# Kernel tuning notes

Hardware: AMD Instinct MI355X
Metric: run time of the kernel (lower is better)

## Reference

```python
import jax, jax.numpy as jnp
import numpy as np

N_NODES = 50000
N_EDGES = 800000


def _sage_conv(h, ei, W_l, W_r, b_l):
    """PyG SAGEConv: lin_l(mean_{j->i} h_j) + lin_r(h_i). lin_l has bias, lin_r does not."""
    src, dst = ei[0], ei[1]
    # mean-aggregate raw features first (linear commutes with mean) to avoid [E, out] intermediates
    msum = jax.ops.segment_sum(h[src], dst, num_segments=N_NODES)          # [N, d]
    cnt = jax.ops.segment_sum(jnp.ones((ei.shape[1], 1), h.dtype), dst,
                              num_segments=N_NODES)                         # [N, 1]
    mean = msum / jnp.maximum(cnt, 1.0)
    return mean @ W_l + b_l + h @ W_r


def setup_inputs() -> dict:
    key = jax.random.key(0)
    ks = jax.random.split(key, 8)
    d_in, d_hid, d_out = 64, 64, 32
    return {
        "x": jax.random.normal(ks[0], (N_NODES, d_in), dtype=jnp.float32),
        "ei0": jax.random.randint(ks[1], (2, N_EDGES), 0, N_NODES, dtype=jnp.int32),
        "ei1": jax.random.randint(ks[2], (2, N_EDGES), 0, N_NODES, dtype=jnp.int32),
        "Wl": jax.random.normal(ks[3], (2, 2, d_in, d_hid), dtype=jnp.float32) * 0.05,
        "Wr": jax.random.normal(ks[4], (2, 2, d_in, d_hid), dtype=jnp.float32) * 0.05,
        "bl": jax.random.normal(ks[5], (2, 2, d_hid), dtype=jnp.float32) * 0.05,
        "lin_W": jax.random.normal(ks[6], (d_hid, d_out), dtype=jnp.float32) * 0.05,
        "lin_b": jax.random.normal(ks[7], (d_out,), dtype=jnp.float32) * 0.05,
    }


def reference(x, ei0, ei1, Wl, Wr, bl, lin_W, lin_b):
    edge_indices = (ei0, ei1)  # one edge_index per relation
    h = x
    for l in range(2):  # layers (structurally fixed)
        out = None
        for r, ei in enumerate(edge_indices):  # HeteroConv aggr='sum' over relations
            y = _sage_conv(h, ei, Wl[l, r], Wr[l, r], bl[l, r])
            out = y if out is None else out + y
        h = jax.nn.relu(out)
    return h @ lin_W + lin_b
```

## Files before the change

### kernel.cpp

```cpp
#include <hip/hip_runtime.h>

#define NN 50000
#define CAP 32
#define OVF_CAP 4096
#define SHARD_W 64
#define NSH 782
#define NPB 512

__device__ __forceinline__ unsigned short f2bf(float f) {
    unsigned u = __float_as_uint(f);
    u += 0x7fffu + ((u >> 16) & 1u);
    return (unsigned short)(u >> 16);
}
__device__ __forceinline__ float bf2f(unsigned short u) {
    return __uint_as_float(((unsigned)u) << 16);
}

__global__ __launch_bounds__(256) void init_fuse(
    const float* __restrict__ in, unsigned short* __restrict__ out, int n4,
    int* __restrict__ zbuf, int nint)
{
    int stride = gridDim.x * blockDim.x;
    int id0 = blockIdx.x * blockDim.x + threadIdx.x;
    for (int i = id0; i < n4; i += stride) {
        float4 v = ((const float4*)in)[i];
        ushort4 o;
        o.x = f2bf(v.x); o.y = f2bf(v.y); o.z = f2bf(v.z); o.w = f2bf(v.w);
        ((ushort4*)out)[i] = o;
    }
    for (int i = id0; i < nint; i += stride) zbuf[i] = 0;
}


__global__ __launch_bounds__(256) void shard_hist(
    const int* __restrict__ ei0, int E0,
    const int* __restrict__ ei1, int E1,
    unsigned short* __restrict__ hist16)
{
    __shared__ unsigned lh[NSH];
    int local = blockIdx.x; int rel = 0;
    if (local >= NPB) { local -= NPB; rel = 1; }
    int pb = (local & 7) * (NPB / 8) + (local >> 3);
    const int* ei = rel ? ei1 : ei0;
    int E         = rel ? E1  : E0;
    int ce = (E + NPB - 1) / NPB;
    int lo = pb * ce, hi = min(lo + ce, E);

    for (int i = threadIdx.x; i < NSH; i += 256) lh[i] = 0;
    __syncthreads();
    for (int t = lo + threadIdx.x; t < hi; t += 256)
        atomicAdd(&lh[ei[E + t] >> 6], 1u);
    __syncthreads();
    for (int i = threadIdx.x; i < NSH; i += 256)
        hist16[((size_t)rel * NSH + i) * NPB + pb] = (unsigned short)lh[i];
}

__global__ __launch_bounds__(256) void total_pass(
    const unsigned short* __restrict__ hist16, int* __restrict__ tot)
{
    int gw = (blockIdx.x * 256 + threadIdx.x) >> 6;
    int lane = threadIdx.x & 63;
    if (gw >= 2 * NSH) return;
    uint4 v = ((const uint4*)(hist16 + (size_t)gw * NPB))[lane];
    unsigned s = (v.x & 0xffffu) + (v.x >> 16) + (v.y & 0xffffu) + (v.y >> 16)
               + (v.z & 0xffffu) + (v.z >> 16) + (v.w & 0xffffu) + (v.w >> 16);
    for (int off = 32; off; off >>= 1) s += __shfl_down(s, off);
    if (lane == 0) tot[gw] = (int)s;
}

__global__ __launch_bounds__(256) void scan_pass(
    const int* __restrict__ tot, int* __restrict__ sbase)
{
    __shared__ int ps[256];
    int t = threadIdx.x;
    int v[7];
    int s = 0;
    #pragma unroll
    for (int j = 0; j < 7; j++) {
        int i = t * 7 + j;
        v[j] = (i < 2 * NSH) ? tot[i] : 0;
        s += v[j];
    }
    ps[t] = s;
    __syncthreads();
    for (int off = 1; off < 256; off <<= 1) {
        int add = (t >= off) ? ps[t - off] : 0;
        __syncthreads();
        ps[t] += add;
        __syncthreads();
    }
    int run = (t == 0) ? 0 : ps[t - 1];
    #pragma unroll
    for (int j = 0; j < 7; j++) {
        int i = t * 7 + j;
        if (i < 2 * NSH) sbase[i] = run;
        run += v[j];
    }
    if (t == 255) sbase[2 * NSH] = run;
}

__global__ __launch_bounds__(256) void blockbase_pass(
    const unsigned short* __restrict__ hist16, const int* __restrict__ sbase,
    unsigned* __restrict__ pbase)
{
    int gw = (blockIdx.x * 256 + threadIdx.x) >> 6;
    int lane = threadIdx.x & 63;
    if (gw >= 2 * NSH) return;
    uint4 v = ((const uint4*)(hist16 + (size_t)gw * NPB))[lane];
    unsigned c[8] = {v.x & 0xffffu, v.x >> 16, v.y & 0xffffu, v.y >> 16,
                     v.z & 0xffffu, v.z >> 16, v.w & 0xffffu, v.w >> 16};
    unsigned lsum = 0;
    #pragma unroll
    for (int j = 0; j < 8; j++) lsum += c[j];
    unsigned incl = lsum;
    for (int off = 1; off < 64; off <<= 1) {
        unsigned n = __shfl_up(incl, off);
        if (lane >= off) incl += n;
    }
    unsigned run = (unsigned)sbase[gw] + incl - lsum;
    unsigned* prow = pbase + (size_t)gw * NPB + lane * 8;
    #pragma unroll
    for (int j = 0; j < 8; j++) { prow[j] = run; run += c[j]; }
}

__global__ __launch_bounds__(256) void partition_pass(
    const int* __restrict__ ei0, int E0,
    const int* __restrict__ ei1, int E1,
    const unsigned* __restrict__ pbase,
    unsigned* __restrict__ compact)
{
    __shared__ unsigned lbase[NSH];
    __shared__ unsigned lrank[NSH];
    int local = blockIdx.x; int rel = 0;
    if (local >= NPB) { local -= NPB; rel = 1; }
    int pb = (local & 7) * (NPB / 8) + (local >> 3);
    const int* ei = rel ? ei1 : ei0;
    int E         = rel ? E1  : E0;
    int ce = (E + NPB - 1) / NPB;
    int lo = pb * ce, hi = min(lo + ce, E);

    for (int i = threadIdx.x; i < NSH; i += 256) {
        lbase[i] = pbase[((size_t)rel * NSH + i) * NPB + pb];
        lrank[i] = 0;
    }
    __syncthreads();
    for (int t = lo + threadIdx.x; t < hi; t += 256) {
        int dst = ei[E + t];
        int src = ei[t];
        int s = dst >> 6;
        unsigned r = atomicAdd(&lrank[s], 1u);
        compact[lbase[s] + r] = ((unsigned)dst << 16) | (unsigned)src;
    }
}

__global__ __launch_bounds__(256) void bin_pass(
    const unsigned* __restrict__ compact, const int* __restrict__ sbase,
    unsigned short* __restrict__ bins, int* __restrict__ deg,
    int2* __restrict__ ovf, int* __restrict__ ovf_cnt)
{
    __shared__ unsigned lcnt[SHARD_W];
    int bid = blockIdx.x;
    int rel = bid / NSH;
    int s   = bid - rel * NSH;
    if (threadIdx.x < SHARD_W) lcnt[threadIdx.x] = 0;
    __syncthreads();
    int base = sbase[bid];
    int tot  = sbase[bid + 1] - base;
    int taskbase = rel * NN + s * SHARD_W;
    for (int j = threadIdx.x; j < tot; j += 256) {
        unsigned e = compact[base + j];
        int dst = (int)(e >> 16);
        int src = (int)(e & 0xffffu);
        int loc = dst & (SHARD_W - 1);
        unsigned r = atomicAdd(&lcnt[loc], 1u);
        int task = taskbase + loc;
        if (r < CAP) {
            bins[(size_t)task * CAP + r] = (unsigned short)src;
        } else {
            int o = atomicAdd(ovf_cnt, 1);
            if (o < OVF_CAP) ovf[o] = make_int2(task, src);
        }
    }
    __syncthreads();
    if (threadIdx.x < SHARD_W) {
        int node = s * SHARD_W + threadIdx.x;
        if (node < NN) deg[rel * NN + node] = (int)lcnt[threadIdx.x];
    }
}

__global__ __launch_bounds__(256) void aggregate(
    const unsigned short* __restrict__ bins, const int* __restrict__ deg,
    const unsigned short* __restrict__ hb, unsigned short* __restrict__ agg,
    const int2* __restrict__ ovf, const int* __restrict__ ovf_cnt)
{
    int lane = threadIdx.x & 63;
    int half = lane >> 5;
    int p = lane & 31;
    int wid = (blockIdx.x * blockDim.x + threadIdx.x) >> 6;
    int nwaves = (gridDim.x * blockDim.x) >> 6;
    const unsigned int* hb32 = (const unsigned int*)hb;
    unsigned int* agg32 = (unsigned int*)agg;

    for (int task = wid; task < 2 * NN; task += nwaves) {
        int d = deg[task];
        int m = min(d, CAP);
        int idx = 0;
        if (lane < m) idx = bins[(size_t)task * CAP + lane];
        float a00=0.f,a01=0.f, a10=0.f,a11=0.f, a20=0.f,a21=0.f, a30=0.f,a31=0.f;
        int F = m >> 1;
        int q = 0;
        for (; q + 4 <= F; q += 4) {
            int s0 = __shfl(idx, 2*(q+0) + half);
            int s1 = __shfl(idx, 2*(q+1) + half);
            int s2 = __shfl(idx, 2*(q+2) + half);
            int s3 = __shfl(idx, 2*(q+3) + half);
            unsigned u0 = hb32[(size_t)s0 * 32 + p];
            unsigned u1 = hb32[(size_t)s1 * 32 + p];
            unsigned u2 = hb32[(size_t)s2 * 32 + p];
            unsigned u3 = hb32[(size_t)s3 * 32 + p];
            a00 += __uint_as_float(u0 << 16); a01 += __uint_as_float(u0 & 0xffff0000u);
            a10 += __uint_as_float(u1 << 16); a11 += __uint_as_float(u1 & 0xffff0000u);
            a20 += __uint_as_float(u2 << 16); a21 += __uint_as_float(u2 & 0xffff0000u);
            a30 += __uint_as_float(u3 << 16); a31 += __uint_as_float(u3 & 0xffff0000u);
        }
        for (; q < F; ++q) {
            int s = __shfl(idx, 2*q + half);
            unsigned u = hb32[(size_t)s * 32 + p];
            a00 += __uint_as_float(u << 16); a01 += __uint_as_float(u & 0xffff0000u);
        }
        if (m & 1) {
            int s = __shfl(idx, m - 1);
            if (half == 0) {
                unsigned u = hb32[(size_t)s * 32 + p];
                a00 += __uint_as_float(u << 16); a01 += __uint_as_float(u & 0xffff0000u);
            }
        }
        if (d > CAP) {
            int cnt = min(*ovf_cnt, OVF_CAP);
            for (int e = 0; e < cnt; ++e) {
                int2 v = ovf[e];
                if (v.x == task && half == 0) {
                    unsigned u = hb32[(size_t)v.y * 32 + p];
                    a00 += __uint_as_float(u << 16); a01 += __uint_as_float(u & 0xffff0000u);
                }
            }
        }
        float s0 = (a00 + a10) + (a20 + a30);
        float s1 = (a01 + a11) + (a21 + a31);
        s0 += __shfl_xor(s0, 32);
        s1 += __shfl_xor(s1, 32);
        if (half == 0) {
            float inv = 1.0f / (float)max(d, 1);
            unsigned lo = (unsigned)f2bf(s0 * inv);
            unsigned hi = (unsigned)f2bf(s1 * inv);
            agg32[(size_t)task * 32 + p] = lo | (hi << 16);
        }
    }
}

#define RST 66
__global__ __launch_bounds__(256) void layer_gemm(
    const unsigned short* __restrict__ agg0, const unsigned short* __restrict__ agg1,
    const unsigned short* __restrict__ selfb,
    const float* __restrict__ Wl0, const float* __restrict__ Wl1,
    const float* __restrict__ Wr0, const float* __restrict__ Wr1,
    const float* __restrict__ b0, const float* __restrict__ b1,
    unsigned short* __restrict__ hb16)
{
    __shared__ float Wch[64 * 64];
    __shared__ float rowsT[64 * RST];
    __shared__ float bias[64];

    int tid = threadIdx.x;
    int base = blockIdx.x * 64;
    if (tid < 64) bias[tid] = b0[tid] + b1[tid];

    int j8 = (tid & 7) * 8;
    int n2 = (tid >> 3) * 2;

    float acc[2][8];
    #pragma unroll
    for (int i = 0; i < 2; i++)
        #pragma unroll
        for (int c = 0; c < 8; c++) acc[i][c] = 0.f;

    for (int chunk = 0; chunk < 3; chunk++) {
        const float* W = (chunk == 0) ? Wl0 : (chunk == 1) ? Wl1 : Wr0;
        const unsigned short* src = (chunk == 0) ? agg0 : (chunk == 1) ? agg1 : selfb;
        __syncthreads();
        #pragma unroll
        for (int r = 0; r < 4; r++) {
            int i = tid + 256 * r;
            float4 w = *(const float4*)&W[i * 4];
            if (chunk == 2) {
                float4 w2 = *(const float4*)&Wr1[i * 4];
                w.x += w2.x; w.y += w2.y; w.z += w2.z; w.w += w2.w;
            }
            *(float4*)&Wch[i * 4] = w;
        }
        #pragma unroll
        for (int r = 0; r < 4; r++) {
            int i = tid + 256 * r;
            int node = i >> 4;
            int k4 = (i & 15) * 4;
            int g = base + node;
            ushort4 u = make_ushort4(0, 0, 0, 0);
            if (g < NN) u = *(const ushort4*)&src[(size_t)g * 64 + k4];
            rowsT[(k4 + 0) * RST + node] = bf2f(u.x);
            rowsT[(k4 + 1) * RST + node] = bf2f(u.y);
            rowsT[(k4 + 2) * RST + node] = bf2f(u.z);
            rowsT[(k4 + 3) * RST + node] = bf2f(u.w);
        }
        __syncthreads();
        #pragma unroll 4
        for (int k = 0; k < 64; k++) {
            float4 wa = *(const float4*)&Wch[k * 64 + j8];
            float4 wb = *(const float4*)&Wch[k * 64 + j8 + 4];
            float2 rv = *(const float2*)&rowsT[k * RST + n2];
            float w[8] = {wa.x, wa.y, wa.z, wa.w, wb.x, wb.y, wb.z, wb.w};
            float rr[2] = {rv.x, rv.y};
            #pragma unroll
            for (int i = 0; i < 2; i++)
                #pragma unroll
                for (int c = 0; c < 8; c++)
                    acc[i][c] = fmaf(rr[i], w[c], acc[i][c]);
        }
    }

    #pragma unroll
    for (int i = 0; i < 2; i++) {
        int g = base + n2 + i;
        if (g < NN) {
            ushort4 p0, p1;
            p0.x = f2bf(fmaxf(acc[i][0] + bias[j8 + 0], 0.f));
            p0.y = f2bf(fmaxf(acc[i][1] + bias[j8 + 1], 0.f));
            p0.z = f2bf(fmaxf(acc[i][2] + bias[j8 + 2], 0.f));
            p0.w = f2bf(fmaxf(acc[i][3] + bias[j8 + 3], 0.f));
            p1.x = f2bf(fmaxf(acc[i][4] + bias[j8 + 4], 0.f));
            p1.y = f2bf(fmaxf(acc[i][5] + bias[j8 + 5], 0.f));
            p1.z = f2bf(fmaxf(acc[i][6] + bias[j8 + 6], 0.f));
            p1.w = f2bf(fmaxf(acc[i][7] + bias[j8 + 7], 0.f));
            *(ushort4*)&hb16[(size_t)g * 64 + j8]     = p0;
            *(ushort4*)&hb16[(size_t)g * 64 + j8 + 4] = p1;
        }
    }
}

__global__ __launch_bounds__(256) void layer_gemm_final(
    const unsigned short* __restrict__ agg0, const unsigned short* __restrict__ agg1,
    const unsigned short* __restrict__ selfb,
    const float* __restrict__ Wl0, const float* __restrict__ Wl1,
    const float* __restrict__ Wr0, const float* __restrict__ Wr1,
    const float* __restrict__ b0, const float* __restrict__ b1,
    const float* __restrict__ linW, const float* __restrict__ linb,
    float* __restrict__ out)
{
    __shared__ float Wch[64 * 64];
    __shared__ float rowsT[64 * RST];
    __shared__ float bias[64];

    int tid = threadIdx.x;
    int base = blockIdx.x * 64;
    if (tid < 64) bias[tid] = b0[tid] + b1[tid];

    int j8 = (tid & 7) * 8;
    int n2 = (tid >> 3) * 2;

    float acc[2][8];
    #pragma unroll
    for (int i = 0; i < 2; i++)
        #pragma unroll
        for (int c = 0; c < 8; c++) acc[i][c] = 0.f;

    for (int chunk = 0; chunk < 3; chunk++) {
        const float* W = (chunk == 0) ? Wl0 : (chunk == 1) ? Wl1 : Wr0;
        const unsigned short* src = (chunk == 0) ? agg0 : (chunk == 1) ? agg1 : selfb;
        __syncthreads();
        #pragma unroll
        for (int r = 0; r < 4; r++) {
            int i = tid + 256 * r;
            float4 w = *(const float4*)&W[i * 4];
            if (chunk == 2) {
                float4 w2 = *(const float4*)&Wr1[i * 4];
                w.x += w2.x; w.y += w2.y; w.z += w2.z; w.w += w2.w;
            }
            *(float4*)&Wch[i * 4] = w;
        }
        #pragma unroll
        for (int r = 0; r < 4; r++) {
            int i = tid + 256 * r;
            int node = i >> 4;
            int k4 = (i & 15) * 4;
            int g = base + node;
            ushort4 u = make_ushort4(0, 0, 0, 0);
            if (g < NN) u = *(const ushort4*)&src[(size_t)g * 64 + k4];
            rowsT[(k4 + 0) * RST + node] = bf2f(u.x);
            rowsT[(k4 + 1) * RST + node] = bf2f(u.y);
            rowsT[(k4 + 2) * RST + node] = bf2f(u.z);
            rowsT[(k4 + 3) * RST + node] = bf2f(u.w);
        }
        __syncthreads();
        #pragma unroll 4
        for (int k = 0; k < 64; k++) {
            float4 wa = *(const float4*)&Wch[k * 64 + j8];
            float4 wb = *(const float4*)&Wch[k * 64 + j8 + 4];
            float2 rv = *(const float2*)&rowsT[k * RST + n2];
            float w[8] = {wa.x, wa.y, wa.z, wa.w, wb.x, wb.y, wb.z, wb.w};
            float rr[2] = {rv.x, rv.y};
            #pragma unroll
            for (int i = 0; i < 2; i++)
                #pragma unroll
                for (int c = 0; c < 8; c++)
                    acc[i][c] = fmaf(rr[i], w[c], acc[i][c]);
        }
    }

    float o[2][8];
    #pragma unroll
    for (int i = 0; i < 2; i++)
        #pragma unroll
        for (int c = 0; c < 8; c++)
            o[i][c] = fmaxf(acc[i][c] + bias[j8 + c], 0.f);

    __syncthreads();

    #pragma unroll
    for (int r = 0; r < 2; r++) {
        int i = tid + 256 * r;
        *(float4*)&Wch[i * 4] = *(const float4*)&linW[i * 4];
    }
    if (tid < 32) bias[tid] = linb[tid];
    #pragma unroll
    for (int i = 0; i < 2; i++)
        #pragma unroll
        for (int c = 0; c < 8; c++)
            rowsT[(j8 + c) * RST + (n2 + i)] = o[i][c];
    __syncthreads();

    int j4 = (tid & 7) * 4;
    float acc2[2][4];
    #pragma unroll
    for (int i = 0; i < 2; i++)
        #pragma unroll
        for (int c = 0; c < 4; c++) acc2[i][c] = 0.f;
    #pragma unroll 4
    for (int k = 0; k < 64; k++) {
        float4 w = *(const float4*)&Wch[k * 32 + j4];
        float2 rv = *(const float2*)&rowsT[k * RST + n2];
        float wr[4] = {w.x, w.y, w.z, w.w};
        float rr[2] = {rv.x, rv.y};
        #pragma unroll
        for (int i = 0; i < 2; i++)
            #pragma unroll
            for (int c = 0; c < 4; c++)
                acc2[i][c] = fmaf(rr[i], wr[c], acc2[i][c]);
    }
    #pragma unroll
    for (int i = 0; i < 2; i++) {
        int g = base + n2 + i;
        if (g < NN) {
            float4 ov;
            ov.x = acc2[i][0] + bias[j4 + 0];
            ov.y = acc2[i][1] + bias[j4 + 1];
            ov.z = acc2[i][2] + bias[j4 + 2];
            ov.w = acc2[i][3] + bias[j4 + 3];
            *(float4*)&out[(size_t)g * 32 + j4] = ov;
        }
    }
}

extern "C" void kernel_launch(void* const* d_in, const int* in_sizes, int n_in,
                              void* d_out, int out_size, void* d_ws, size_t ws_size,
                              hipStream_t stream)
{
    const float* x    = (const float*)d_in[0];
    const int*   ei0  = (const int*)d_in[1];
    const int*   ei1  = (const int*)d_in[2];
    const float* Wl   = (const float*)d_in[3];
    const float* Wr   = (const float*)d_in[4];
    const float* bl   = (const float*)d_in[5];
    const float* linW = (const float*)d_in[6];
    const float* linb = (const float*)d_in[7];
    float* out = (float*)d_out;

    int E0 = in_sizes[1] / 2;
    int E1 = in_sizes[2] / 2;

    unsigned short* bins = (unsigned short*)d_ws;
    unsigned short* h1b  = bins + (size_t)2 * NN * CAP;
    unsigned short* aggb = h1b + (size_t)NN * 64;
    unsigned short* agg0 = aggb;
    unsigned short* agg1 = aggb + (size_t)NN * 64;
    unsigned short* xb   = aggb + (size_t)2 * NN * 64;
    int*  deg     = (int*)(xb + (size_t)NN * 64);
    int*  ovf_cnt = deg + 2 * NN;
    int2* ovf     = (int2*)(ovf_cnt + 8);

    unsigned*       compact = (unsigned*)h1b;
    unsigned short* hist16  = aggb;
    unsigned*       pbase   = (unsigned*)(aggb + (size_t)2 * NSH * NPB);
    int*            tot     = (int*)(aggb + (size_t)2 * NSH * NPB * 3);
    int*            sbase   = tot + 2 * NSH;

    dim3 blk(256);
    int ggrid = (NN + 63) / 64;
    int wave_grid = (2 * NSH * 64 + 255) / 256;

    init_fuse<<<1024, blk, 0, stream>>>(x, xb, NN * 16, ovf_cnt, 8);

    shard_hist<<<2 * NPB, blk, 0, stream>>>(ei0, E0, ei1, E1, hist16);
    total_pass<<<wave_grid, blk, 0, stream>>>(hist16, tot);
    scan_pass<<<1, blk, 0, stream>>>(tot, sbase);
    blockbase_pass<<<wave_grid, blk, 0, stream>>>(hist16, sbase, pbase);
    partition_pass<<<2 * NPB, blk, 0, stream>>>(ei0, E0, ei1, E1, pbase, compact);
    bin_pass<<<2 * NSH, blk, 0, stream>>>(compact, sbase, bins, deg, ovf, ovf_cnt);

    aggregate<<<4096, blk, 0, stream>>>(bins, deg, xb, aggb, ovf, ovf_cnt);
    layer_gemm<<<ggrid, blk, 0, stream>>>(agg0, agg1, xb,
        Wl + 0, Wl + 4096, Wr + 0, Wr + 4096, bl + 0, bl + 64, h1b);

    aggregate<<<4096, blk, 0, stream>>>(bins, deg, h1b, aggb, ovf, ovf_cnt);
    layer_gemm_final<<<ggrid, blk, 0, stream>>>(agg0, agg1, h1b,
        Wl + 8192, Wl + 12288, Wr + 8192, Wr + 12288, bl + 128, bl + 192,
        linW, linb, out);
}
```

Baseline: 245.8 us.

## Fuse binning preprocessing passes into one cooperative kernel with grid syncs

Merges the seven preprocessing kernels (bf16 conversion, histogram, totals, scan, block bases, partition, binning) into a single cooperative launch of 1024 blocks, with grid.sync() between phases. The aim is to remove the per-launch overhead and inter-kernel gaps of many small kernels. In exchange, each phase runs with a fixed grid (the bin phase loops over shards, total/blockbase use only part of the grid), the single-block scan leaves the rest of the grid idle at a barrier, and all 1024 blocks must be co-resident for the cooperative launch.

```diff
diff --git a/kernel.cpp b/kernel.cpp
--- a/kernel.cpp
+++ b/kernel.cpp
@@ -1,4 +1,7 @@
 #include <hip/hip_runtime.h>
+#include <hip/hip_cooperative_groups.h>
+
+namespace cg = cooperative_groups;
 
 #define NN 50000
 #define CAP 32
@@ -16,175 +19,173 @@
     return __uint_as_float(((unsigned)u) << 16);
 }
 
-__global__ __launch_bounds__(256) void init_fuse(
-    const float* __restrict__ in, unsigned short* __restrict__ out, int n4,
-    int* __restrict__ zbuf, int nint)
-{
-    int stride = gridDim.x * blockDim.x;
-    int id0 = blockIdx.x * blockDim.x + threadIdx.x;
-    for (int i = id0; i < n4; i += stride) {
-        float4 v = ((const float4*)in)[i];
-        ushort4 o;
-        o.x = f2bf(v.x); o.y = f2bf(v.y); o.z = f2bf(v.z); o.w = f2bf(v.w);
-        ((ushort4*)out)[i] = o;
-    }
-    for (int i = id0; i < nint; i += stride) zbuf[i] = 0;
-}
-
-
-__global__ __launch_bounds__(256) void shard_hist(
+__global__ __launch_bounds__(256) void binning_coop(
+    const float* __restrict__ x, unsigned short* __restrict__ xb,
     const int* __restrict__ ei0, int E0,
     const int* __restrict__ ei1, int E1,
-    unsigned short* __restrict__ hist16)
-{
-    __shared__ unsigned lh[NSH];
-    int local = blockIdx.x; int rel = 0;
-    if (local >= NPB) { local -= NPB; rel = 1; }
-    int pb = (local & 7) * (NPB / 8) + (local >> 3);
-    const int* ei = rel ? ei1 : ei0;
-    int E         = rel ? E1  : E0;
-    int ce = (E + NPB - 1) / NPB;
-    int lo = pb * ce, hi = min(lo + ce, E);
-
-    for (int i = threadIdx.x; i < NSH; i += 256) lh[i] = 0;
-    __syncthreads();
-    for (int t = lo + threadIdx.x; t < hi; t += 256)
-        atomicAdd(&lh[ei[E + t] >> 6], 1u);
-    __syncthreads();
-    for (int i = threadIdx.x; i < NSH; i += 256)
-        hist16[((size_t)rel * NSH + i) * NPB + pb] = (unsigned short)lh[i];
-}
-
-__global__ __launch_bounds__(256) void total_pass(
-    const unsigned short* __restrict__ hist16, int* __restrict__ tot)
-{
-    int gw = (blockIdx.x * 256 + threadIdx.x) >> 6;
-    int lane = threadIdx.x & 63;
-    if (gw >= 2 * NSH) return;
-    uint4 v = ((const uint4*)(hist16 + (size_t)gw * NPB))[lane];
-    unsigned s = (v.x & 0xffffu) + (v.x >> 16) + (v.y & 0xffffu) + (v.y >> 16)
-               + (v.z & 0xffffu) + (v.z >> 16) + (v.w & 0xffffu) + (v.w >> 16);
-    for (int off = 32; off; off >>= 1) s += __shfl_down(s, off);
-    if (lane == 0) tot[gw] = (int)s;
-}
-
-__global__ __launch_bounds__(256) void scan_pass(
-    const int* __restrict__ tot, int* __restrict__ sbase)
-{
-    __shared__ int ps[256];
-    int t = threadIdx.x;
-    int v[7];
-    int s = 0;
-    #pragma unroll
-    for (int j = 0; j < 7; j++) {
-        int i = t * 7 + j;
-        v[j] = (i < 2 * NSH) ? tot[i] : 0;
-        s += v[j];
-    }
-    ps[t] = s;
-    __syncthreads();
-    for (int off = 1; off < 256; off <<= 1) {
-        int add = (t >= off) ? ps[t - off] : 0;
-        __syncthreads();
-        ps[t] += add;
-        __syncthreads();
-    }
-    int run = (t == 0) ? 0 : ps[t - 1];
-    #pragma unroll
-    for (int j = 0; j < 7; j++) {
-        int i = t * 7 + j;
-        if (i < 2 * NSH) sbase[i] = run;
-        run += v[j];
-    }
-    if (t == 255) sbase[2 * NSH] = run;
-}
-
-__global__ __launch_bounds__(256) void blockbase_pass(
-    const unsigned short* __restrict__ hist16, const int* __restrict__ sbase,
-    unsigned* __restrict__ pbase)
-{
-    int gw = (blockIdx.x * 256 + threadIdx.x) >> 6;
-    int lane = threadIdx.x & 63;
-    if (gw >= 2 * NSH) return;
-    uint4 v = ((const uint4*)(hist16 + (size_t)gw * NPB))[lane];
-    unsigned c[8] = {v.x & 0xffffu, v.x >> 16, v.y & 0xffffu, v.y >> 16,
-                     v.z & 0xffffu, v.z >> 16, v.w & 0xffffu, v.w >> 16};
-    unsigned lsum = 0;
-    #pragma unroll
-    for (int j = 0; j < 8; j++) lsum += c[j];
-    unsigned incl = lsum;
-    for (int off = 1; off < 64; off <<= 1) {
-        unsigned n = __shfl_up(incl, off);
-        if (lane >= off) incl += n;
-    }
-    unsigned run = (unsigned)sbase[gw] + incl - lsum;
-    unsigned* prow = pbase + (size_t)gw * NPB + lane * 8;
-    #pragma unroll
-    for (int j = 0; j < 8; j++) { prow[j] = run; run += c[j]; }
-}
-
-__global__ __launch_bounds__(256) void partition_pass(
-    const int* __restrict__ ei0, int E0,
-    const int* __restrict__ ei1, int E1,
-    const unsigned* __restrict__ pbase,
-    unsigned* __restrict__ compact)
-{
-    __shared__ unsigned lbase[NSH];
-    __shared__ unsigned lrank[NSH];
-    int local = blockIdx.x; int rel = 0;
-    if (local >= NPB) { local -= NPB; rel = 1; }
-    int pb = (local & 7) * (NPB / 8) + (local >> 3);
-    const int* ei = rel ? ei1 : ei0;
-    int E         = rel ? E1  : E0;
-    int ce = (E + NPB - 1) / NPB;
-    int lo = pb * ce, hi = min(lo + ce, E);
-
-    for (int i = threadIdx.x; i < NSH; i += 256) {
-        lbase[i] = pbase[((size_t)rel * NSH + i) * NPB + pb];
-        lrank[i] = 0;
-    }
-    __syncthreads();
-    for (int t = lo + threadIdx.x; t < hi; t += 256) {
-        int dst = ei[E + t];
-        int src = ei[t];
-        int s = dst >> 6;
-        unsigned r = atomicAdd(&lrank[s], 1u);
-        compact[lbase[s] + r] = ((unsigned)dst << 16) | (unsigned)src;
-    }
-}
-
-__global__ __launch_bounds__(256) void bin_pass(
-    const unsigned* __restrict__ compact, const int* __restrict__ sbase,
+    unsigned short* __restrict__ hist16,
+    int* __restrict__ tot, int* __restrict__ sbase,
+    unsigned* __restrict__ pbase,
+    unsigned* __restrict__ compact,
     unsigned short* __restrict__ bins, int* __restrict__ deg,
     int2* __restrict__ ovf, int* __restrict__ ovf_cnt)
 {
-    __shared__ unsigned lcnt[SHARD_W];
-    int bid = blockIdx.x;
-    int rel = bid / NSH;
-    int s   = bid - rel * NSH;
-    if (threadIdx.x < SHARD_W) lcnt[threadIdx.x] = 0;
-    __syncthreads();
-    int base = sbase[bid];
-    int tot  = sbase[bid + 1] - base;
-    int taskbase = rel * NN + s * SHARD_W;
-    for (int j = threadIdx.x; j < tot; j += 256) {
-        unsigned e = compact[base + j];
-        int dst = (int)(e >> 16);
-        int src = (int)(e & 0xffffu);
-        int loc = dst & (SHARD_W - 1);
-        unsigned r = atomicAdd(&lcnt[loc], 1u);
-        int task = taskbase + loc;
-        if (r < CAP) {
-            bins[(size_t)task * CAP + r] = (unsigned short)src;
-        } else {
-            int o = atomicAdd(ovf_cnt, 1);
-            if (o < OVF_CAP) ovf[o] = make_int2(task, src);
-        }
-    }
-    __syncthreads();
-    if (threadIdx.x < SHARD_W) {
-        int node = s * SHARD_W + threadIdx.x;
-        if (node < NN) deg[rel * NN + node] = (int)lcnt[threadIdx.x];
+    cg::grid_group grid = cg::this_grid();
+    __shared__ unsigned sh[2 * NSH];
+    int tid  = threadIdx.x;
+    int gtid = blockIdx.x * 256 + tid;
+    int gsz  = gridDim.x * 256;
+
+    for (int i = gtid; i < NN * 16; i += gsz) {
+        float4 v = ((const float4*)x)[i];
+        ushort4 o;
+        o.x = f2bf(v.x); o.y = f2bf(v.y); o.z = f2bf(v.z); o.w = f2bf(v.w);
+        ((ushort4*)xb)[i] = o;
+    }
+    if (gtid < 8) ovf_cnt[gtid] = 0;
+
+    {
+        unsigned* lh = sh;
+        int local = blockIdx.x; int rel = 0;
+        if (local >= NPB) { local -= NPB; rel = 1; }
+        int pb = (local & 7) * (NPB / 8) + (local >> 3);
+        const int* ei = rel ? ei1 : ei0;
+        int E         = rel ? E1  : E0;
+        int ce = (E + NPB - 1) / NPB;
+        int lo = pb * ce, hi = min(lo + ce, E);
+        for (int i = tid; i < NSH; i += 256) lh[i] = 0;
+        __syncthreads();
+        for (int t = lo + tid; t < hi; t += 256)
+            atomicAdd(&lh[ei[E + t] >> 6], 1u);
+        __syncthreads();
+        for (int i = tid; i < NSH; i += 256)
+            hist16[((size_t)rel * NSH + i) * NPB + pb] = (unsigned short)lh[i];
+    }
+    grid.sync();
+
+    {
+        int gw = gtid >> 6;
+        int lane = tid & 63;
+        if (gw < 2 * NSH) {
+            uint4 v = ((const uint4*)(hist16 + (size_t)gw * NPB))[lane];
+            unsigned s = (v.x & 0xffffu) + (v.x >> 16) + (v.y & 0xffffu) + (v.y >> 16)
+                       + (v.z & 0xffffu) + (v.z >> 16) + (v.w & 0xffffu) + (v.w >> 16);
+            for (int off = 32; off; off >>= 1) s += __shfl_down(s, off);
+            if (lane == 0) tot[gw] = (int)s;
+        }
+    }
+    grid.sync();
+
+    if (blockIdx.x == 0) {
+        int* ps = (int*)sh;
+        int t = tid;
+        int v[7];
+        int s = 0;
+        #pragma unroll
+        for (int j = 0; j < 7; j++) {
+            int i = t * 7 + j;
+            v[j] = (i < 2 * NSH) ? tot[i] : 0;
+            s += v[j];
+        }
+        ps[t] = s;
+        __syncthreads();
+        for (int off = 1; off < 256; off <<= 1) {
+            int add = (t >= off) ? ps[t - off] : 0;
+            __syncthreads();
+            ps[t] += add;
+            __syncthreads();
+        }
+        int run = (t == 0) ? 0 : ps[t - 1];
+        #pragma unroll
+        for (int j = 0; j < 7; j++) {
+            int i = t * 7 + j;
+            if (i < 2 * NSH) sbase[i] = run;
+            run += v[j];
+        }
+        if (t == 255) sbase[2 * NSH] = run;
+    }
+    grid.sync();
+
+    {
+        int gw = gtid >> 6;
+        int lane = tid & 63;
+        if (gw < 2 * NSH) {
+            uint4 v = ((const uint4*)(hist16 + (size_t)gw * NPB))[lane];
+            unsigned c[8] = {v.x & 0xffffu, v.x >> 16, v.y & 0xffffu, v.y >> 16,
+                             v.z & 0xffffu, v.z >> 16, v.w & 0xffffu, v.w >> 16};
+            unsigned lsum = 0;
+            #pragma unroll
+            for (int j = 0; j < 8; j++) lsum += c[j];
+            unsigned incl = lsum;
+            for (int off = 1; off < 64; off <<= 1) {
+                unsigned n = __shfl_up(incl, off);
+                if (lane >= off) incl += n;
+            }
+            unsigned run = (unsigned)sbase[gw] + incl - lsum;
+            unsigned* prow = pbase + (size_t)gw * NPB + lane * 8;
+            #pragma unroll
+            for (int j = 0; j < 8; j++) { prow[j] = run; run += c[j]; }
+        }
+    }
+    grid.sync();
+
+    {
+        unsigned* lbase = sh;
+        unsigned* lrank = sh + NSH;
+        int local = blockIdx.x; int rel = 0;
+        if (local >= NPB) { local -= NPB; rel = 1; }
+        int pb = (local & 7) * (NPB / 8) + (local >> 3);
+        const int* ei = rel ? ei1 : ei0;
+        int E         = rel ? E1  : E0;
+        int ce = (E + NPB - 1) / NPB;
+        int lo = pb * ce, hi = min(lo + ce, E);
+        __syncthreads();
+        for (int i = tid; i < NSH; i += 256) {
+            lbase[i] = pbase[((size_t)rel * NSH + i) * NPB + pb];
+            lrank[i] = 0;
+        }
+        __syncthreads();
+        for (int t = lo + tid; t < hi; t += 256) {
+            int dst = ei[E + t];
+            int src = ei[t];
+            int s = dst >> 6;
+            unsigned r = atomicAdd(&lrank[s], 1u);
+            compact[lbase[s] + r] = ((unsigned)dst << 16) | (unsigned)src;
+        }
+    }
+    grid.sync();
+
+    {
+        unsigned* lcnt = sh;
+        for (int bid = blockIdx.x; bid < 2 * NSH; bid += gridDim.x) {
+            if (tid < SHARD_W) lcnt[tid] = 0;
+            __syncthreads();
+            int rel = bid / NSH;
+            int s   = bid - rel * NSH;
+            int base = sbase[bid];
+            int tt   = sbase[bid + 1] - base;
+            int taskbase = rel * NN + s * SHARD_W;
+            for (int j = tid; j < tt; j += 256) {
+                unsigned e = compact[base + j];
+                int dst = (int)(e >> 16);
+                int src = (int)(e & 0xffffu);
+                int loc = dst & (SHARD_W - 1);
+                unsigned r = atomicAdd(&lcnt[loc], 1u);
+                int task = taskbase + loc;
+                if (r < CAP) {
+                    bins[(size_t)task * CAP + r] = (unsigned short)src;
+                } else {
+                    int o = atomicAdd(ovf_cnt, 1);
+                    if (o < OVF_CAP) ovf[o] = make_int2(task, src);
+                }
+            }
+            __syncthreads();
+            if (tid < SHARD_W) {
+                int node = s * SHARD_W + tid;
+                if (node < NN) deg[rel * NN + node] = (int)lcnt[tid];
+            }
+            __syncthreads();
+        }
     }
 }
 
@@ -504,16 +505,14 @@
 
     dim3 blk(256);
     int ggrid = (NN + 63) / 64;
-    int wave_grid = (2 * NSH * 64 + 255) / 256;
-
-    init_fuse<<<1024, blk, 0, stream>>>(x, xb, NN * 16, ovf_cnt, 8);
-
-    shard_hist<<<2 * NPB, blk, 0, stream>>>(ei0, E0, ei1, E1, hist16);
-    total_pass<<<wave_grid, blk, 0, stream>>>(hist16, tot);
-    scan_pass<<<1, blk, 0, stream>>>(tot, sbase);
-    blockbase_pass<<<wave_grid, blk, 0, stream>>>(hist16, sbase, pbase);
-    partition_pass<<<2 * NPB, blk, 0, stream>>>(ei0, E0, ei1, E1, pbase, compact);
-    bin_pass<<<2 * NSH, blk, 0, stream>>>(compact, sbase, bins, deg, ovf, ovf_cnt);
+
+    void* kargs[] = {
+        (void*)&x, (void*)&xb, (void*)&ei0, (void*)&E0, (void*)&ei1, (void*)&E1,
+        (void*)&hist16, (void*)&tot, (void*)&sbase, (void*)&pbase,
+        (void*)&compact, (void*)&bins, (void*)&deg, (void*)&ovf, (void*)&ovf_cnt
+    };
+    hipLaunchCooperativeKernel((void*)binning_coop, dim3(2 * NPB), blk,
+                               kargs, 0, stream);
 
     aggregate<<<4096, blk, 0, stream>>>(bins, deg, xb, aggb, ovf, ovf_cnt);
     layer_gemm<<<ggrid, blk, 0, stream>>>(agg0, agg1, xb,
```

Measured after the change: 797.9 us. +224.6%, slower.
